# Optimization experiments

Hardware: AMD Instinct MI355X
Metric: run time of the kernel (lower is better)

The kernel has to match this reference:

```python
import jax, jax.numpy as jnp
import numpy as np

B, I, O, D = 8, 16, 16, 512
BASIS = 5

def setup_inputs() -> dict:
    key = jax.random.key(0)
    k1, k2, k3 = jax.random.split(key, 3)
    x = jax.random.normal(k1, (B, I, D), dtype=jnp.float32)
    fan_in = BASIS * I  # kaiming_uniform(a=sqrt(5)) on (O, 5I, 1, 1) -> bound = 1/sqrt(fan_in)
    bound = 1.0 / np.sqrt(fan_in)
    weight = jax.random.uniform(k2, (O, BASIS * I), dtype=jnp.float32, minval=-bound, maxval=bound)
    bias = jax.random.uniform(k3, (O,), dtype=jnp.float32, minval=-bound, maxval=bound)
    return {"x": x, "weight": weight, "bias": bias}

def reference(x, weight, bias):
    # x: (B, I, D); weight: (O, 5*I); bias: (O,)
    # Equivariant 1->2 basis ops (normalize=False), fused with the 1x1-conv channel
    # contraction instead of materializing the (B, 5I, D, D) concat:
    #   op1 = diag_embed(x); op2 = row-broadcast(x); op3 = col-broadcast(x);
    #   op4 = diag_embed(sum(x)); op5 = full-broadcast(sum(x))
    b_, i_, d_ = x.shape
    o_ = weight.shape[0]
    w = weight.reshape(o_, BASIS, i_)  # channel layout of the concat: [op1|op2|op3|op4|op5]
    s = x.sum(axis=-1)                                     # (B, I)
    y1 = jnp.einsum('oi,bid->bod', w[:, 0], x)             # diagonal term
    y2 = jnp.einsum('oi,bid->bod', w[:, 1], x)             # row broadcast term
    y3 = jnp.einsum('oi,bid->bod', w[:, 2], x)             # col broadcast term
    y4 = jnp.einsum('oi,bi->bo', w[:, 3], s)               # sum on diagonal
    y5 = jnp.einsum('oi,bi->bo', w[:, 4], s)               # sum everywhere
    out = y2[..., :, None] + y3[..., None, :] + y5[..., None, None]  # (B, O, D, D)
    diag = y1 + y4[..., None]                              # (B, O, D)
    out = out + jnp.eye(d_, dtype=x.dtype) * diag[..., :, None]
    return out + bias[None, :, None, None]
```

## Files before the change

### kernel.cpp

```cpp
#include <hip/hip_runtime.h>

#define NB 8
#define NI 16
#define NO 16
#define ND 512
#define ROWS 32
#define RT   (ND / ROWS)

__global__ __launch_bounds__(256) void leq_fused(
    const float* __restrict__ x, const float* __restrict__ weight,
    const float* __restrict__ bias, float4* __restrict__ out)
{
    const int blk = blockIdx.x;
    const int rt  = blk & (RT - 1);
    const int bo  = blk >> 4;
    const int b   = bo >> 4;
    const int o   = bo & 15;
    const int t   = threadIdx.x;

    __shared__ __align__(16) float colvS[ND];
    __shared__ float rowfS[ND];
    __shared__ float diagfS[ND];
    __shared__ float rwS[ROWS], dgS[ROWS];
    __shared__ float red4[4], red5[4];

    const float* wbase = weight + o * (5 * NI);
    const float* xb    = x + b * (NI * ND);

    const int d0 = t, d1 = t + 256;
    float a1a = 0.f, a2a = 0.f, a3a = 0.f;
    float a1b = 0.f, a2b = 0.f, a3b = 0.f;
    float p4 = 0.f, p5 = 0.f;

    #pragma unroll
    for (int i = 0; i < NI; ++i) {
        const float w0 = wbase[0 * NI + i];
        const float w1 = wbase[1 * NI + i];
        const float w2 = wbase[2 * NI + i];
        const float w3 = wbase[3 * NI + i];
        const float w4 = wbase[4 * NI + i];
        const float xa = xb[i * ND + d0];
        const float xc = xb[i * ND + d1];
        a1a += w0 * xa; a2a += w1 * xa; a3a += w2 * xa;
        a1b += w0 * xc; a2b += w1 * xc; a3b += w2 * xc;
        const float xs = xa + xc;
        p4 += w3 * xs; p5 += w4 * xs;
    }
    colvS[d0]  = a3a; colvS[d1]  = a3b;
    rowfS[d0]  = a2a; rowfS[d1]  = a2b;
    diagfS[d0] = a1a; diagfS[d1] = a1b;

    #pragma unroll
    for (int off = 32; off > 0; off >>= 1) {
        p4 += __shfl_down(p4, off, 64);
        p5 += __shfl_down(p5, off, 64);
    }
    const int wave = t >> 6, lane = t & 63;
    if (lane == 0) { red4[wave] = p4; red5[wave] = p5; }
    __syncthreads();

    const float y4 = red4[0] + red4[1] + red4[2] + red4[3];
    const float y5 = red5[0] + red5[1] + red5[2] + red5[3];
    const float base = y5 + bias[o];
    if (t < ROWS) {
        const int r = rt * ROWS + t;
        rwS[t] = rowfS[r] + base;
        dgS[t] = diagfS[r] + y4;
    }
    __syncthreads();

    const float4* colv4 = reinterpret_cast<const float4*>(colvS);
    const int out_base = bo * (ND * (ND / 4)) + rt * ROWS * (ND / 4);

    #pragma unroll 4
    for (int k = 0; k < ROWS * (ND / 4) / 256; ++k) {
        const int idx = k * 256 + t;
        const int c4  = idx & 127;
        const int rl  = idx >> 7;
        const int r   = rt * ROWS + rl;

        const float  rv = rwS[rl];
        const float  dv = dgS[rl];
        const float4 cv = colv4[c4];

        const int dcol = r - (c4 << 2);
        float4 res;
        res.x = rv + cv.x + ((dcol == 0) ? dv : 0.0f);
        res.y = rv + cv.y + ((dcol == 1) ? dv : 0.0f);
        res.z = rv + cv.z + ((dcol == 2) ? dv : 0.0f);
        res.w = rv + cv.w + ((dcol == 3) ? dv : 0.0f);
        out[out_base + idx] = res;
    }
}

extern "C" void kernel_launch(void* const* d_in, const int* in_sizes, int n_in,
                              void* d_out, int out_size, void* d_ws, size_t ws_size,
                              hipStream_t stream) {
    const float* x      = (const float*)d_in[0];
    const float* weight = (const float*)d_in[1];
    const float* bias   = (const float*)d_in[2];

    leq_fused<<<NB * NO * RT, 256, 0, stream>>>(x, weight, bias, (float4*)d_out);
}
```

Measured before the change: 27.49 us.

## Enlarge row tiles, vectorize channel contraction, and use nontemporal output stores

```diff
diff --git a/kernel.cpp b/kernel.cpp
--- a/kernel.cpp
+++ b/kernel.cpp
@@ -4,51 +4,60 @@
 #define NI 16
 #define NO 16
 #define ND 512
-#define ROWS 32
+#define ROWS 128
 #define RT   (ND / ROWS)
+
+typedef float f32x4 __attribute__((ext_vector_type(4)));
 
 __global__ __launch_bounds__(256) void leq_fused(
     const float* __restrict__ x, const float* __restrict__ weight,
-    const float* __restrict__ bias, float4* __restrict__ out)
+    const float* __restrict__ bias, f32x4* __restrict__ out)
 {
     const int blk = blockIdx.x;
     const int rt  = blk & (RT - 1);
-    const int bo  = blk >> 4;
+    const int bo  = blk >> 2;
     const int b   = bo >> 4;
     const int o   = bo & 15;
     const int t   = threadIdx.x;
 
     __shared__ __align__(16) float colvS[ND];
-    __shared__ float rowfS[ND];
-    __shared__ float diagfS[ND];
+    __shared__ __align__(16) float part1[ND];
+    __shared__ __align__(16) float part2[ND];
+    __shared__ __align__(16) float part3[ND];
     __shared__ float rwS[ROWS], dgS[ROWS];
     __shared__ float red4[4], red5[4];
 
     const float* wbase = weight + o * (5 * NI);
     const float* xb    = x + b * (NI * ND);
+    const float  bia   = bias[o];
 
-    const int d0 = t, d1 = t + 256;
-    float a1a = 0.f, a2a = 0.f, a3a = 0.f;
-    float a1b = 0.f, a2b = 0.f, a3b = 0.f;
+    const int half = t >> 7;
+    const int fq   = t & 127;
+
+    f32x4 a1 = {0,0,0,0}, a2 = {0,0,0,0}, a3 = {0,0,0,0};
     float p4 = 0.f, p5 = 0.f;
 
     #pragma unroll
-    for (int i = 0; i < NI; ++i) {
+    for (int i2 = 0; i2 < NI / 2; ++i2) {
+        const int   i  = i2 * 2 + half;
         const float w0 = wbase[0 * NI + i];
         const float w1 = wbase[1 * NI + i];
         const float w2 = wbase[2 * NI + i];
         const float w3 = wbase[3 * NI + i];
         const float w4 = wbase[4 * NI + i];
-        const float xa = xb[i * ND + d0];
-        const float xc = xb[i * ND + d1];
-        a1a += w0 * xa; a2a += w1 * xa; a3a += w2 * xa;
-        a1b += w0 * xc; a2b += w1 * xc; a3b += w2 * xc;
-        const float xs = xa + xc;
+        const f32x4 xv = reinterpret_cast<const f32x4*>(xb + i * ND)[fq];
+        a1 += w0 * xv;
+        a2 += w1 * xv;
+        a3 += w2 * xv;
+        const float xs = xv.x + xv.y + xv.z + xv.w;
         p4 += w3 * xs; p5 += w4 * xs;
     }
-    colvS[d0]  = a3a; colvS[d1]  = a3b;
-    rowfS[d0]  = a2a; rowfS[d1]  = a2b;
-    diagfS[d0] = a1a; diagfS[d1] = a1b;
+
+    if (half) {
+        reinterpret_cast<f32x4*>(part1)[fq] = a1;
+        reinterpret_cast<f32x4*>(part2)[fq] = a2;
+        reinterpret_cast<f32x4*>(part3)[fq] = a3;
+    }
 
     #pragma unroll
     for (int off = 32; off > 0; off >>= 1) {
@@ -59,17 +68,32 @@
     if (lane == 0) { red4[wave] = p4; red5[wave] = p5; }
     __syncthreads();
 
-    const float y4 = red4[0] + red4[1] + red4[2] + red4[3];
-    const float y5 = red5[0] + red5[1] + red5[2] + red5[3];
-    const float base = y5 + bias[o];
-    if (t < ROWS) {
-        const int r = rt * ROWS + t;
-        rwS[t] = rowfS[r] + base;
-        dgS[t] = diagfS[r] + y4;
+    const float y4   = red4[0] + red4[1] + red4[2] + red4[3];
+    const float y5   = red5[0] + red5[1] + red5[2] + red5[3];
+    const float base = y5 + bia;
+
+    if (half == 0) {
+        const f32x4 o1 = reinterpret_cast<const f32x4*>(part1)[fq];
+        const f32x4 o2 = reinterpret_cast<const f32x4*>(part2)[fq];
+        const f32x4 o3 = reinterpret_cast<const f32x4*>(part3)[fq];
+        reinterpret_cast<f32x4*>(colvS)[fq] = a3 + o3;
+        if ((fq >> 5) == rt) {
+            const int rl4 = (fq & 31) << 2;
+            const f32x4 rw = a2 + o2;
+            const f32x4 dg = a1 + o1;
+            rwS[rl4 + 0] = rw.x + base;
+            rwS[rl4 + 1] = rw.y + base;
+            rwS[rl4 + 2] = rw.z + base;
+            rwS[rl4 + 3] = rw.w + base;
+            dgS[rl4 + 0] = dg.x + y4;
+            dgS[rl4 + 1] = dg.y + y4;
+            dgS[rl4 + 2] = dg.z + y4;
+            dgS[rl4 + 3] = dg.w + y4;
+        }
     }
     __syncthreads();
 
-    const float4* colv4 = reinterpret_cast<const float4*>(colvS);
+    const f32x4* colv4 = reinterpret_cast<const f32x4*>(colvS);
     const int out_base = bo * (ND * (ND / 4)) + rt * ROWS * (ND / 4);
 
     #pragma unroll 4
@@ -81,15 +105,15 @@
 
         const float  rv = rwS[rl];
         const float  dv = dgS[rl];
-        const float4 cv = colv4[c4];
+        const f32x4  cv = colv4[c4];
 
         const int dcol = r - (c4 << 2);
-        float4 res;
+        f32x4 res;
         res.x = rv + cv.x + ((dcol == 0) ? dv : 0.0f);
         res.y = rv + cv.y + ((dcol == 1) ? dv : 0.0f);
         res.z = rv + cv.z + ((dcol == 2) ? dv : 0.0f);
         res.w = rv + cv.w + ((dcol == 3) ? dv : 0.0f);
-        out[out_base + idx] = res;
+        __builtin_nontemporal_store(res, &out[out_base + idx]);
     }
 }
 
@@ -100,5 +124,5 @@
     const float* weight = (const float*)d_in[1];
     const float* bias   = (const float*)d_in[2];
 
-    leq_fused<<<NB * NO * RT, 256, 0, stream>>>(x, weight, bias, (float4*)d_out);
+    leq_fused<<<NB * NO * RT, 256, 0, stream>>>(x, weight, bias, (f32x4*)d_out);
 }
```

Result: slower. 30.67 us (+11.6%).
